# Kernel tuning notes

Hardware: AMD Instinct MI355X
Metric: run time of the kernel (lower is better)

The kernel has to match this reference:

```python
import jax, jax.numpy as jnp
import numpy as np

B, S, D_IN, D_ST = 4, 4096, 1024, 1024


def setup_inputs() -> dict:
    key = jax.random.key(0)
    ks = jax.random.split(key, 7)
    s_in = 1.0 / np.sqrt(D_IN)
    s_st = 1.0 / np.sqrt(D_ST)
    return {
        "x": jax.random.normal(ks[0], (B, S, D_IN), dtype=jnp.float32),
        "gate_w": jax.random.uniform(ks[1], (D_IN, D_ST), jnp.float32, -s_in, s_in),
        "gate_b": jax.random.uniform(ks[2], (D_ST,), jnp.float32, -s_in, s_in),
        "inp_w": jax.random.uniform(ks[3], (D_IN, D_ST), jnp.float32, -s_in, s_in),
        "inp_b": jax.random.uniform(ks[4], (D_ST,), jnp.float32, -s_in, s_in),
        "out_w": jax.random.uniform(ks[5], (D_ST, D_IN), jnp.float32, -s_st, s_st),
        "out_b": jax.random.uniform(ks[6], (D_IN,), jnp.float32, -s_st, s_st),
    }


def reference(x, gate_w, gate_b, inp_w, inp_b, out_w, out_b):
    # x: [B, S, D_in]
    inp = jnp.einsum("bsd,de->bse", x, inp_w) + inp_b      # [B,S,Dst]
    gate = jax.nn.sigmoid(jnp.einsum("bsd,de->bse", x, gate_w) + gate_b)
    b_t = (1.0 - gate) * inp                               # [B,S,Dst]

    # affine recurrence h_t = gate_t * h_{t-1} + b_t via lax.scan over time
    def step(h, ab):
        a, b = ab
        h = a * h + b
        return h, h

    a_sb = jnp.swapaxes(gate, 0, 1)  # [S,B,Dst]
    b_sb = jnp.swapaxes(b_t, 0, 1)
    h0 = jnp.zeros((x.shape[0], inp.shape[-1]), dtype=x.dtype)
    _, hs = jax.lax.scan(step, h0, (a_sb, b_sb))           # [S,B,Dst]
    scan_out = jnp.swapaxes(hs, 0, 1)                      # [B,S,Dst]

    return x + jnp.einsum("bse,ed->bsd", scan_out, out_w) + out_b
```

## Files before the change

kernel.cpp:

```cpp
#include <hip/hip_runtime.h>

typedef unsigned short u16;
typedef unsigned int   u32;
typedef __bf16 bf16x8 __attribute__((ext_vector_type(8)));
typedef float  f32x4  __attribute__((ext_vector_type(4)));

#define DEVI __device__ __forceinline__

DEVI u16 f2bf(float f) {
    union { float f; u32 u; } c; c.f = f;
    u32 u = c.u;
    u32 r = (u + 0x7fffu + ((u >> 16) & 1u)) >> 16;
    return (u16)r;
}
DEVI float bf2f(u16 v) {
    union { u32 u; float f; } c; c.u = ((u32)v) << 16;
    return c.f;
}

DEVI void gload16(const void* g, void* l) {
    __builtin_amdgcn_global_load_lds(
        (const __attribute__((address_space(1))) void*)g,
        (__attribute__((address_space(3))) void*)l, 16, 0, 0);
}


#define VMW(N)  asm volatile("s_waitcnt vmcnt(" #N ")" ::: "memory")
#define BAR     __builtin_amdgcn_s_barrier()
#define MMP     BAR; asm volatile("s_waitcnt lgkmcnt(0)" ::: "memory"); \
                __builtin_amdgcn_sched_barrier(0); __builtin_amdgcn_s_setprio(1)
#define MME     __builtin_amdgcn_s_setprio(0); BAR
#define MMEV(N) __builtin_amdgcn_s_setprio(0); VMW(N); BAR

DEVI void stage_kh(const u16* g, u16* slot, int tid) {
    const int K = 1024;
    const int wvb = (tid >> 6) << 9;
    const int r = tid >> 2;
    const int p = tid & 3;
    const int c = p ^ (r & 3);
    const long off = (long)r * K + (c << 3);
    gload16(g + off, slot + wvb);
    gload16(g + off + (long)128 * K, slot + 4096 + wvb);
}

DEVI void lda4(bf16x8 a[4], const u16* base, int mh) {
#pragma unroll
    for (int q = 0; q < 4; ++q)
        a[q] = *(const bf16x8*)(base + mh * 2048 + q * 512);
}
DEVI void ldb4(bf16x8 b[4], const u16* base) {
#pragma unroll
    for (int n = 0; n < 4; ++n)
        b[n] = *(const bf16x8*)(base + n * 512);
}
DEVI void mm16(f32x4 (&acc)[8][4], const bf16x8 a[4], const bf16x8 b[4], int mh) {
#pragma unroll
    for (int q = 0; q < 4; ++q)
#pragma unroll
        for (int n = 0; n < 4; ++n)
            acc[mh * 4 + q][n] =
                __builtin_amdgcn_mfma_f32_16x16x32_bf16(a[q], b[n], acc[mh * 4 + q][n], 0, 0, 0);
}

DEVI void pipeline(const u16* Ablk, const u16* Bblk, u16* lds,
                   f32x4 (&acc)[8][4], int tid) {
    const int lane = tid & 63;
    const int wm = (tid >> 6) >> 2, wn = (tid >> 6) & 3;
    const int pchunk = ((lane >> 4) ^ (lane & 3)) << 3;
    const int aoff = wm * 4096 + (lane & 15) * 32 + pchunk;
    const int boff = 16384 + wn * 2048 + (lane & 15) * 32 + pchunk;
    u16* b0 = lds;
    u16* b1 = lds + 32768;

    stage_kh(Bblk,      b0 + 16384, tid);
    stage_kh(Ablk,      b0,         tid);
    stage_kh(Bblk + 32, b0 + 24576, tid);
    stage_kh(Ablk + 32, b0 + 8192,  tid);
    stage_kh(Bblk + 64, b1 + 16384, tid);
    stage_kh(Ablk + 64, b1,         tid);
    stage_kh(Bblk + 96, b1 + 24576, tid);
    VMW(10); BAR;

    bf16x8 af[4], bfr[4];

#pragma unroll 1
    for (int j = 0; j < 7; ++j) {
        const u16* Aod = Ablk + (2 * j + 1) * 64;
        const u16* At2 = Ablk + (2 * j + 2) * 64;
        const u16* Bt2 = Bblk + (2 * j + 2) * 64;
        lda4(af, b0 + aoff, 0); ldb4(bfr, b0 + boff);
        stage_kh(Aod + 32, b1 + 8192, tid);
        MMP; mm16(acc, af, bfr, 0); MME;
        lda4(af, b0 + aoff, 1);
        stage_kh(Bt2, b0 + 16384, tid);
        MMP; mm16(acc, af, bfr, 1); MMEV(10);
        lda4(af, b0 + 8192 + aoff, 0); ldb4(bfr, b0 + 8192 + boff);
        stage_kh(At2, b0, tid);
        MMP; mm16(acc, af, bfr, 0); MME;
        lda4(af, b0 + 8192 + aoff, 1);
        stage_kh(Bt2 + 32, b0 + 24576, tid);
        MMP; mm16(acc, af, bfr, 1); MMEV(10);
        lda4(af, b1 + aoff, 0); ldb4(bfr, b1 + boff);
        stage_kh(At2 + 32, b0 + 8192, tid);
        MMP; mm16(acc, af, bfr, 0); MME;
        lda4(af, b1 + aoff, 1);
        stage_kh(Bt2 + 64, b1 + 16384, tid);
        MMP; mm16(acc, af, bfr, 1); MMEV(10);
        lda4(af, b1 + 8192 + aoff, 0); ldb4(bfr, b1 + 8192 + boff);
        stage_kh(At2 + 64, b1, tid);
        MMP; mm16(acc, af, bfr, 0); MME;
        lda4(af, b1 + 8192 + aoff, 1);
        stage_kh(Bt2 + 96, b1 + 24576, tid);
        MMP; mm16(acc, af, bfr, 1); MMEV(10);
    }
    {
        const u16* Aod = Ablk + 15 * 64;
        lda4(af, b0 + aoff, 0); ldb4(bfr, b0 + boff);
        stage_kh(Aod + 32, b1 + 8192, tid);
        MMP; mm16(acc, af, bfr, 0); MME;
        lda4(af, b0 + aoff, 1);
        MMP; mm16(acc, af, bfr, 1); MMEV(8);
        lda4(af, b0 + 8192 + aoff, 0); ldb4(bfr, b0 + 8192 + boff);
        MMP; mm16(acc, af, bfr, 0); MME;
        lda4(af, b0 + 8192 + aoff, 1);
        MMP; mm16(acc, af, bfr, 1); MMEV(4);
        lda4(af, b1 + aoff, 0); ldb4(bfr, b1 + boff);
        MMP; mm16(acc, af, bfr, 0); MME;
        lda4(af, b1 + aoff, 1);
        MMP; mm16(acc, af, bfr, 1); MMEV(0);
        lda4(af, b1 + 8192 + aoff, 0); ldb4(bfr, b1 + 8192 + boff);
        MMP; mm16(acc, af, bfr, 0); MME;
        lda4(af, b1 + 8192 + aoff, 1);
        MMP; mm16(acc, af, bfr, 1); MME;
    }
}


__global__ __launch_bounds__(512, 2) void k_gemm_cat8(
    const u16* __restrict__ A, const u16* __restrict__ Bcat,
    const float* __restrict__ gb, const float* __restrict__ ib,
    u32* __restrict__ ab) {
    __shared__ __align__(16) u16 lds[65536];
    const int tid = threadIdx.x, lane = tid & 63;
    const int wm = (tid >> 6) >> 2, wn = (tid >> 6) & 3;

    int fid = (int)blockIdx.y * 8 + (int)blockIdx.x;
    int swz = (fid & 7) * 64 + (fid >> 3);
    const long bn = swz & 7, bm = swz >> 3;

    f32x4 acc[8][4] = {};
    pipeline(A + bm * 256 * 1024, Bcat + bn * 256 * 1024, lds, acc, tid);

    const long rbase = bm * 256 + wm * 128;
    const int chbase = (int)bn * 128 + wn * 32;
#pragma unroll
    for (int t = 0; t < 2; ++t) {
        int ch = chbase + t * 16 + (lane & 15);
        float g0 = gb[ch], i0 = ib[ch];
#pragma unroll
        for (int m = 0; m < 8; ++m) {
            long row = rbase + m * 16 + ((lane >> 4) << 2);
#pragma unroll
            for (int i = 0; i < 4; ++i) {
                float pg = acc[m][2 * t][i] + g0;
                float pi = acc[m][2 * t + 1][i] + i0;
                float aa = 1.0f / (1.0f + __expf(-pg));
                float bb = (1.0f - aa) * pi;
                ab[(row + i) * 1024 + ch] = (u32)f2bf(aa) | ((u32)f2bf(bb) << 16);
            }
        }
    }
}


__global__ __launch_bounds__(512, 2) void k_gemm_out8(
    const u16* __restrict__ A, const u16* __restrict__ Bt,
    const float* __restrict__ xres, const float* __restrict__ ob,
    float* __restrict__ out) {
    __shared__ __align__(16) u16 lds[65536];
    const int tid = threadIdx.x, lane = tid & 63;
    const int wm = (tid >> 6) >> 2, wn = (tid >> 6) & 3;

    int fid = (int)blockIdx.y * 4 + (int)blockIdx.x;
    int swz = (fid & 7) * 32 + (fid >> 3);
    const long bn = swz & 3, bm = swz >> 2;

    f32x4 acc[8][4] = {};
    pipeline(A + bm * 256 * 1024, Bt + bn * 256 * 1024, lds, acc, tid);

    const long rbase = bm * 256 + wm * 128;
    const int cbase = (int)bn * 256 + wn * 64;
#pragma unroll
    for (int n = 0; n < 4; ++n) {
        int col = cbase + n * 16 + (lane & 15);
        float o0 = ob[col];
#pragma unroll
        for (int m = 0; m < 8; ++m) {
            long row = rbase + m * 16 + ((lane >> 4) << 2);
#pragma unroll
            for (int i = 0; i < 4; ++i) {
                long o = (row + i) * 1024 + col;
                out[o] = acc[m][n][i] + o0 + xres[o];
            }
        }
    }
}


__global__ __launch_bounds__(256) void k_cvt_x(const float4* __restrict__ x,
                                               uint2* __restrict__ o, int n4) {
    int i = blockIdx.x * 256 + threadIdx.x;
    if (i < n4) {
        float4 v = x[i];
        uint2 r;
        r.x = (u32)f2bf(v.x) | ((u32)f2bf(v.y) << 16);
        r.y = (u32)f2bf(v.z) | ((u32)f2bf(v.w) << 16);
        o[i] = r;
    }
}

__global__ __launch_bounds__(256) void k_transpose_bf(const float* __restrict__ w,
                                                      u16* __restrict__ wt, int R, int C) {
    __shared__ float t[32][33];
    int c0 = blockIdx.x * 32, r0 = blockIdx.y * 32;
    int x = threadIdx.x & 31, y = threadIdx.x >> 5;
    for (int i = y; i < 32; i += 8) t[i][x] = w[(size_t)(r0 + i) * C + c0 + x];
    __syncthreads();
    for (int i = y; i < 32; i += 8) wt[(size_t)(c0 + i) * R + r0 + x] = f2bf(t[x][i]);
}

__global__ __launch_bounds__(256) void k_transpose_cat(const float* __restrict__ gw,
                                                       const float* __restrict__ iw,
                                                       u16* __restrict__ wt, int K, int C) {
    __shared__ float t[32][33];
    int c0 = blockIdx.x * 32, r0 = blockIdx.y * 32;
    const float* w = blockIdx.z ? iw : gw;
    int x = threadIdx.x & 31, y = threadIdx.x >> 5;
    for (int i = y; i < 32; i += 8) t[i][x] = w[(size_t)(r0 + i) * C + c0 + x];
    __syncthreads();
    for (int i = y; i < 32; i += 8) {
        int ch = c0 + i;
        int r = ((ch >> 4) << 5) | ((int)blockIdx.z << 4) | (ch & 15);
        wt[(size_t)r * K + r0 + x] = f2bf(t[x][i]);
    }
}


__global__ __launch_bounds__(256) void k_scanA(const u32* __restrict__ ab,
                                               float2* __restrict__ cAB) {
    int e = blockIdx.x * 256 + threadIdx.x;
    int c = blockIdx.y, bt = blockIdx.z;
    long base = ((long)bt * 4096 + c * 64) * 1024 + e;
    float Aa = 1.f, H = 0.f;
#pragma unroll 4
    for (int i = 0; i < 64; ++i) {
        u32 v = ab[base + (long)i * 1024];
        float a = bf2f((u16)v), b = bf2f((u16)(v >> 16));
        H = a * H + b;
        Aa *= a;
    }
    cAB[((long)bt * 64 + c) * 1024 + e] = make_float2(Aa, H);
}

__global__ __launch_bounds__(256) void k_scanB(const float2* __restrict__ cAB,
                                               float* __restrict__ hin) {
    int e = blockIdx.x * 256 + threadIdx.x;
    int bt = blockIdx.y;
    float H = 0.f;
#pragma unroll
    for (int c = 0; c < 64; ++c) {
        long s = ((long)bt * 64 + c) * 1024 + e;
        hin[s] = H;
        float2 v = cAB[s];
        H = v.x * H + v.y;
    }
}

__global__ __launch_bounds__(256) void k_scanC(const u32* __restrict__ ab,
                                               const float* __restrict__ hin,
                                               u16* __restrict__ hout) {
    int e = blockIdx.x * 256 + threadIdx.x;
    int c = blockIdx.y, bt = blockIdx.z;
    long base = ((long)bt * 4096 + c * 64) * 1024 + e;
    float H = hin[((long)bt * 64 + c) * 1024 + e];
#pragma unroll 4
    for (int i = 0; i < 64; ++i) {
        u32 v = ab[base + (long)i * 1024];
        H = bf2f((u16)v) * H + bf2f((u16)(v >> 16));
        hout[base + (long)i * 1024] = f2bf(H);
    }
}


extern "C" void kernel_launch(void* const* d_in, const int* in_sizes, int n_in,
                              void* d_out, int out_size, void* d_ws, size_t ws_size,
                              hipStream_t stream) {
    const float* x      = (const float*)d_in[0];
    const float* gate_w = (const float*)d_in[1];
    const float* gate_b = (const float*)d_in[2];
    const float* inp_w  = (const float*)d_in[3];
    const float* inp_b  = (const float*)d_in[4];
    const float* out_w  = (const float*)d_in[5];
    const float* out_b  = (const float*)d_in[6];
    float* out = (float*)d_out;

    const int Bsz = 4, S = 4096, Din = 1024, Dst = 1024;
    const int M = Bsz * S;
    const long nx = (long)M * Din;

    char* w = (char*)d_ws;
    u16* xb      = (u16*)(w);
    u16* catW    = (u16*)(w + 33554432);
    u16* owT     = (u16*)(w + 37748736);
    u16* hbf     = (u16*)(w + 39845888);
    float2* cAB  = (float2*)(w + 73400320);
    float* hin   = (float*)(w + 75497472);

    u32* ab = (u32*)d_out;

    k_cvt_x<<<(int)(nx / 4 / 256), 256, 0, stream>>>((const float4*)x, (uint2*)xb, (int)(nx / 4));
    k_transpose_cat<<<dim3(Dst / 32, Din / 32, 2), 256, 0, stream>>>(gate_w, inp_w, catW, Din, Dst);
    k_transpose_bf<<<dim3(Din / 32, Dst / 32), 256, 0, stream>>>(out_w, owT, Dst, Din);

    k_gemm_cat8<<<dim3(8, M / 256), 512, 0, stream>>>(xb, catW, gate_b, inp_b, ab);

    k_scanA<<<dim3(4, 64, Bsz), 256, 0, stream>>>(ab, cAB);
    k_scanB<<<dim3(4, Bsz), 256, 0, stream>>>(cAB, hin);
    k_scanC<<<dim3(4, 64, Bsz), 256, 0, stream>>>(ab, hin, hbf);

    k_gemm_out8<<<dim3(4, M / 256), 512, 0, stream>>>(hbf, owT, x, out_b, out);
}
```

Baseline: 193.6 us.

## Double-buffer A fragments in registers and drop per-phase pre-MFMA barriers

Restructures the GEMM main loop so A fragments alternate between two register sets (afA/afB), loading the next half-tile from LDS while the current MFMA batch runs. The barrier plus lgkmcnt(0) wait before each MFMA block is removed, leaving one barrier per phase, and vmcnt waits are loosened and rescheduled. This aims to hide LDS read latency and cut synchronisation stalls, at the cost of more VGPRs (a risk at 512 threads with launch bounds of 2 blocks) and a more delicate ordering between LDS overwrites and reads.

```diff
diff --git a/kernel.cpp b/kernel.cpp
--- a/kernel.cpp
+++ b/kernel.cpp
@@ -27,10 +27,10 @@
 
 #define VMW(N)  asm volatile("s_waitcnt vmcnt(" #N ")" ::: "memory")
 #define BAR     __builtin_amdgcn_s_barrier()
-#define MMP     BAR; asm volatile("s_waitcnt lgkmcnt(0)" ::: "memory"); \
-                __builtin_amdgcn_sched_barrier(0); __builtin_amdgcn_s_setprio(1)
-#define MME     __builtin_amdgcn_s_setprio(0); BAR
-#define MMEV(N) __builtin_amdgcn_s_setprio(0); VMW(N); BAR
+#define SP1     __builtin_amdgcn_s_setprio(1)
+#define SP0     __builtin_amdgcn_s_setprio(0)
+#define CLOSE(N) __builtin_amdgcn_sched_barrier(0); VMW(N); BAR
+#define CLOSEB   __builtin_amdgcn_sched_barrier(0); BAR
 
 DEVI void stage_kh(const u16* g, u16* slot, int tid) {
     const int K = 1024;
@@ -43,15 +43,9 @@
     gload16(g + off + (long)128 * K, slot + 4096 + wvb);
 }
 
-DEVI void lda4(bf16x8 a[4], const u16* base, int mh) {
-#pragma unroll
-    for (int q = 0; q < 4; ++q)
-        a[q] = *(const bf16x8*)(base + mh * 2048 + q * 512);
-}
-DEVI void ldb4(bf16x8 b[4], const u16* base) {
-#pragma unroll
-    for (int n = 0; n < 4; ++n)
-        b[n] = *(const bf16x8*)(base + n * 512);
+DEVI void ld4(bf16x8 (&d)[4], const u16* p) {
+#pragma unroll
+    for (int q = 0; q < 4; ++q) d[q] = *(const bf16x8*)(p + q * 512);
 }
 DEVI void mm16(f32x4 (&acc)[8][4], const bf16x8 a[4], const bf16x8 b[4], int mh) {
 #pragma unroll
@@ -66,72 +60,78 @@
                    f32x4 (&acc)[8][4], int tid) {
     const int lane = tid & 63;
     const int wm = (tid >> 6) >> 2, wn = (tid >> 6) & 3;
-    const int pchunk = ((lane >> 4) ^ (lane & 3)) << 3;
-    const int aoff = wm * 4096 + (lane & 15) * 32 + pchunk;
-    const int boff = 16384 + wn * 2048 + (lane & 15) * 32 + pchunk;
-    u16* b0 = lds;
-    u16* b1 = lds + 32768;
-
-    stage_kh(Bblk,      b0 + 16384, tid);
-    stage_kh(Ablk,      b0,         tid);
-    stage_kh(Bblk + 32, b0 + 24576, tid);
-    stage_kh(Ablk + 32, b0 + 8192,  tid);
-    stage_kh(Bblk + 64, b1 + 16384, tid);
-    stage_kh(Ablk + 64, b1,         tid);
-    stage_kh(Bblk + 96, b1 + 24576, tid);
+    const int pch = ((lane >> 4) ^ (lane & 3)) << 3;
+    const int aoff = wm * 4096 + (lane & 15) * 32 + pch;
+    const int boff = wn * 2048 + (lane & 15) * 32 + pch;
+
+    stage_kh(Bblk,      lds + 16384, tid);
+    stage_kh(Ablk,      lds + 0,     tid);
+    stage_kh(Bblk + 32, lds + 24576, tid);
+    stage_kh(Ablk + 32, lds + 8192,  tid);
+    stage_kh(Bblk + 64, lds + 49152, tid);
+    stage_kh(Ablk + 64, lds + 32768, tid);
+    stage_kh(Bblk + 96, lds + 57344, tid);
     VMW(10); BAR;
 
-    bf16x8 af[4], bfr[4];
+    bf16x8 afA[4], afB[4], bfr[4];
+    ld4(afA, lds + aoff);
 
 #pragma unroll 1
     for (int j = 0; j < 7; ++j) {
         const u16* Aod = Ablk + (2 * j + 1) * 64;
         const u16* At2 = Ablk + (2 * j + 2) * 64;
         const u16* Bt2 = Bblk + (2 * j + 2) * 64;
-        lda4(af, b0 + aoff, 0); ldb4(bfr, b0 + boff);
-        stage_kh(Aod + 32, b1 + 8192, tid);
-        MMP; mm16(acc, af, bfr, 0); MME;
-        lda4(af, b0 + aoff, 1);
-        stage_kh(Bt2, b0 + 16384, tid);
-        MMP; mm16(acc, af, bfr, 1); MMEV(10);
-        lda4(af, b0 + 8192 + aoff, 0); ldb4(bfr, b0 + 8192 + boff);
-        stage_kh(At2, b0, tid);
-        MMP; mm16(acc, af, bfr, 0); MME;
-        lda4(af, b0 + 8192 + aoff, 1);
-        stage_kh(Bt2 + 32, b0 + 24576, tid);
-        MMP; mm16(acc, af, bfr, 1); MMEV(10);
-        lda4(af, b1 + aoff, 0); ldb4(bfr, b1 + boff);
-        stage_kh(At2 + 32, b0 + 8192, tid);
-        MMP; mm16(acc, af, bfr, 0); MME;
-        lda4(af, b1 + aoff, 1);
-        stage_kh(Bt2 + 64, b1 + 16384, tid);
-        MMP; mm16(acc, af, bfr, 1); MMEV(10);
-        lda4(af, b1 + 8192 + aoff, 0); ldb4(bfr, b1 + 8192 + boff);
-        stage_kh(At2 + 64, b1, tid);
-        MMP; mm16(acc, af, bfr, 0); MME;
-        lda4(af, b1 + 8192 + aoff, 1);
-        stage_kh(Bt2 + 96, b1 + 24576, tid);
-        MMP; mm16(acc, af, bfr, 1); MMEV(10);
+        ld4(bfr, lds + 16384 + boff);
+        ld4(afB, lds + 2048 + aoff);
+        stage_kh(Aod + 32, lds + 40960, tid);
+        SP1; mm16(acc, afA, bfr, 0); SP0; CLOSE(8);
+        ld4(afA, lds + 8192 + aoff);
+        stage_kh(Bt2, lds + 16384, tid);
+        SP1; mm16(acc, afB, bfr, 1); SP0; CLOSE(8);
+        ld4(bfr, lds + 24576 + boff);
+        ld4(afB, lds + 10240 + aoff);
+        stage_kh(At2, lds + 0, tid);
+        SP1; mm16(acc, afA, bfr, 0); SP0; CLOSE(8);
+        ld4(afA, lds + 32768 + aoff);
+        stage_kh(Bt2 + 32, lds + 24576, tid);
+        SP1; mm16(acc, afB, bfr, 1); SP0; CLOSE(8);
+        ld4(bfr, lds + 49152 + boff);
+        ld4(afB, lds + 34816 + aoff);
+        stage_kh(At2 + 32, lds + 8192, tid);
+        SP1; mm16(acc, afA, bfr, 0); SP0; CLOSE(8);
+        ld4(afA, lds + 40960 + aoff);
+        stage_kh(Bt2 + 64, lds + 49152, tid);
+        SP1; mm16(acc, afB, bfr, 1); SP0; CLOSE(8);
+        ld4(bfr, lds + 57344 + boff);
+        ld4(afB, lds + 43008 + aoff);
+        stage_kh(At2 + 64, lds + 32768, tid);
+        SP1; mm16(acc, afA, bfr, 0); SP0; CLOSE(8);
+        ld4(afA, lds + aoff);
+        stage_kh(Bt2 + 96, lds + 57344, tid);
+        SP1; mm16(acc, afB, bfr, 1); SP0; CLOSE(8);
     }
     {
         const u16* Aod = Ablk + 15 * 64;
-        lda4(af, b0 + aoff, 0); ldb4(bfr, b0 + boff);
-        stage_kh(Aod + 32, b1 + 8192, tid);
-        MMP; mm16(acc, af, bfr, 0); MME;
-        lda4(af, b0 + aoff, 1);
-        MMP; mm16(acc, af, bfr, 1); MMEV(8);
-        lda4(af, b0 + 8192 + aoff, 0); ldb4(bfr, b0 + 8192 + boff);
-        MMP; mm16(acc, af, bfr, 0); MME;
-        lda4(af, b0 + 8192 + aoff, 1);
-        MMP; mm16(acc, af, bfr, 1); MMEV(4);
-        lda4(af, b1 + aoff, 0); ldb4(bfr, b1 + boff);
-        MMP; mm16(acc, af, bfr, 0); MME;
-        lda4(af, b1 + aoff, 1);
-        MMP; mm16(acc, af, bfr, 1); MMEV(0);
-        lda4(af, b1 + 8192 + aoff, 0); ldb4(bfr, b1 + 8192 + boff);
-        MMP; mm16(acc, af, bfr, 0); MME;
-        lda4(af, b1 + 8192 + aoff, 1);
-        MMP; mm16(acc, af, bfr, 1); MME;
+        ld4(bfr, lds + 16384 + boff);
+        ld4(afB, lds + 2048 + aoff);
+        stage_kh(Aod + 32, lds + 40960, tid);
+        SP1; mm16(acc, afA, bfr, 0); SP0; CLOSE(8);
+        ld4(afA, lds + 8192 + aoff);
+        SP1; mm16(acc, afB, bfr, 1); SP0; CLOSEB;
+        ld4(bfr, lds + 24576 + boff);
+        ld4(afB, lds + 10240 + aoff);
+        SP1; mm16(acc, afA, bfr, 0); SP0; CLOSE(4);
+        ld4(afA, lds + 32768 + aoff);
+        SP1; mm16(acc, afB, bfr, 1); SP0; CLOSEB;
+        ld4(bfr, lds + 49152 + boff);
+        ld4(afB, lds + 34816 + aoff);
+        SP1; mm16(acc, afA, bfr, 0); SP0; CLOSE(0);
+        ld4(afA, lds + 40960 + aoff);
+        SP1; mm16(acc, afB, bfr, 1); SP0; CLOSEB;
+        ld4(bfr, lds + 57344 + boff);
+        ld4(afB, lds + 43008 + aoff);
+        SP1; mm16(acc, afA, bfr, 0); SP0; CLOSEB;
+        SP1; mm16(acc, afB, bfr, 1); SP0;
     }
 }
 
```

Result: faster. 184.5 us (-4.7%).
